# Performance work log

Measured on AMD Instinct MI355X. Metric: run time of the kernel, lower is better.

Reference implementation:

```python
import jax, jax.numpy as jnp
import numpy as np

NEG_INF = -9e15  # matches the torch module's zero_vec constant
ALPHA = 0.2      # LeakyReLU negative slope


def setup_inputs() -> dict:
    key = jax.random.key(0)
    k1, k2, k3, k4, k5, k6 = jax.random.split(key, 6)
    N_t, N_o, F_in, F_out = 8192, 8192, 256, 64
    return {
        "t_input": jax.random.normal(k1, (N_t, F_in), dtype=jnp.float32),
        "o_input": jax.random.normal(k2, (N_o, F_in), dtype=jnp.float32),
        "W_t": jax.random.normal(k3, (F_in, F_out), dtype=jnp.float32) * 0.1,
        "W_o": jax.random.normal(k4, (F_in, F_out), dtype=jnp.float32) * 0.1,
        "a": jax.random.normal(k5, (2 * F_out, 1), dtype=jnp.float32) * 0.1,
        "adj": jax.random.randint(k6, (N_t, N_o), 0, 2, dtype=jnp.int32),
    }


def reference(t_input, o_input, W_t, W_o, a, adj):
    # Linear projections
    h_t = t_input @ W_t            # [N_t, F]
    h_o = o_input @ W_o            # [N_o, F]
    F_out = h_t.shape[1]
    a_t = a[:F_out, 0]             # [F]
    a_o = a[F_out:, 0]             # [F]
    # e[i,j] = leakyrelu(cat(h_t[i], h_o[j]) . a) = leakyrelu(h_t[i].a_t + h_o[j].a_o)
    # (avoids materializing the N_t*N_o*2F concat tensor; same math)
    e = jax.nn.leaky_relu(
        (h_t @ a_t)[:, None] + (h_o @ a_o)[None, :], negative_slope=ALPHA
    )                              # [N_t, N_o]
    attention = jnp.where(adj > 0, e, NEG_INF)
    attention = jax.nn.softmax(attention, axis=1)
    # dropout is identity at eval time
    h_prime = attention @ h_o      # [N_t, F]
    return jax.nn.elu(h_prime)     # concat=True
```

## Files before the change

kernel.cpp:

```cpp
#include <hip/hip_runtime.h>
#include <math.h>

#define NT 8192
#define NO 8192
#define FIN 256
#define FOUT 64
#define SPLIT 8
#define JSP (NO/SPLIT)
#define ROWT 64
#define NW32 (NO/32)

#define OFF_ST  ((size_t)0)
#define OFF_SO  (OFF_ST + (size_t)NT)
#define OFF_WT  (OFF_SO + (size_t)NO)
#define OFF_WO  (OFF_WT + (size_t)FIN)
#define OFF_NUM (OFF_WO + (size_t)FIN)
#define OFF_DEN (OFF_NUM + (size_t)SPLIT*NT*FOUT)
#define OFF_HOB (OFF_DEN + (size_t)SPLIT*NT)
#define OFF_ETA (OFF_HOB + (size_t)NO*FOUT/2)
#define OFF_MSK (OFF_ETA + (size_t)NO*2)

typedef __attribute__((ext_vector_type(8))) short short8;
typedef __attribute__((ext_vector_type(4))) float float4v;

static __device__ __forceinline__ unsigned short f2bf(float x) {
  unsigned int u = __float_as_uint(x);
  unsigned int r = (u + 0x7fffu + ((u >> 16) & 1u)) >> 16;
  return (unsigned short)r;
}
static __device__ __forceinline__ int pk2(float a, float b) {
  return (int)((unsigned int)f2bf(a) | ((unsigned int)f2bf(b) << 16));
}
static __device__ __forceinline__ float bflo(int p) {
  return __uint_as_float(((unsigned int)p) << 16);
}
static __device__ __forceinline__ float bfhi(int p) {
  return __uint_as_float(((unsigned int)p) & 0xffff0000u);
}

__global__ void k_mask(const int* __restrict__ adj, float* __restrict__ ws) {
  unsigned int* mw = (unsigned int*)(ws + OFF_MSK);
  int wv = threadIdx.x >> 6, lane = threadIdx.x & 63;
  int gw = blockIdx.x * 4 + wv;
  const int NCH = NT*NO/256;
#pragma unroll 2
  for (int c = gw; c < NCH; c += 8192) {
    int4 a = *(const int4*)(adj + (size_t)c*256 + lane*4);
    unsigned int nib = (a.x > 0 ? 1u : 0u) | (a.y > 0 ? 2u : 0u)
                     | (a.z > 0 ? 4u : 0u) | (a.w > 0 ? 8u : 0u);
    unsigned int val = nib << ((lane & 7) * 4);
    val |= __shfl_xor((int)val, 1, 64);
    val |= __shfl_xor((int)val, 2, 64);
    val |= __shfl_xor((int)val, 4, 64);
    if ((lane & 7) == 0) mw[(size_t)c*8 + (lane >> 3)] = val;
  }
}

__global__ void k_wvec(const float* __restrict__ Wt, const float* __restrict__ Wo,
                       const float* __restrict__ a, float* __restrict__ ws) {
  int k = threadIdx.x;
  float s1 = 0.f, s2 = 0.f;
#pragma unroll
  for (int fq = 0; fq < FOUT/4; ++fq) {
    float4 wt4 = *(const float4*)(Wt + (size_t)k*FOUT + fq*4);
    float4 wo4 = *(const float4*)(Wo + (size_t)k*FOUT + fq*4);
    float4 at4 = *(const float4*)(a + fq*4);
    float4 ao4 = *(const float4*)(a + FOUT + fq*4);
    s1 += wt4.x*at4.x + wt4.y*at4.y + wt4.z*at4.z + wt4.w*at4.w;
    s2 += wo4.x*ao4.x + wo4.y*ao4.y + wo4.z*ao4.z + wo4.w*ao4.w;
  }
  ws[OFF_WT + k] = s1;
  ws[OFF_WO + k] = s2;
}

__global__ void k_st(const float* __restrict__ tin, float* __restrict__ ws) {
  int lane = threadIdx.x & 63;
  int wv   = threadIdx.x >> 6;
  int row  = blockIdx.x * 4 + wv;
  float4 v = ((const float4*)(tin + (size_t)row*FIN))[lane];
  float4 w = ((const float4*)(ws + OFF_WT))[lane];
  float p = v.x*w.x + v.y*w.y + v.z*w.z + v.w*w.w;
#pragma unroll
  for (int m = 32; m >= 1; m >>= 1) p += __shfl_xor(p, m, 64);
  if (lane == 0) ws[OFF_ST + row] = p;
}

__global__ void k_ho(const float* __restrict__ oin, const float* __restrict__ Wo,
                     const float* __restrict__ a, float* __restrict__ ws) {
  unsigned short* hobp = (unsigned short*)(ws + OFF_HOB);
  int lane = threadIdx.x & 63;
  int wv = __builtin_amdgcn_readfirstlane(threadIdx.x >> 6);
  int r0 = blockIdx.x * 16 + wv * 4;
  const float* ob = oin + (size_t)r0 * FIN;
  float acc[4];
#pragma unroll
  for (int r = 0; r < 4; ++r) acc[r] = 0.f;
#pragma unroll 2
  for (int k = 0; k < FIN; k += 4) {
    float w0 = Wo[(size_t)(k+0)*FOUT + lane];
    float w1 = Wo[(size_t)(k+1)*FOUT + lane];
    float w2 = Wo[(size_t)(k+2)*FOUT + lane];
    float w3 = Wo[(size_t)(k+3)*FOUT + lane];
#pragma unroll
    for (int r = 0; r < 4; ++r) {
      float4 ov = *(const float4*)(ob + (size_t)r*FIN + k);
      acc[r] = fmaf(ov.x, w0, acc[r]);
      acc[r] = fmaf(ov.y, w1, acc[r]);
      acc[r] = fmaf(ov.z, w2, acc[r]);
      acc[r] = fmaf(ov.w, w3, acc[r]);
    }
  }
  float ao = a[FOUT + lane];
  int fg = lane >> 4, n16 = lane & 15;
#pragma unroll
  for (int r = 0; r < 4; ++r) {
    int j = r0 + r;
    int jt = j >> 5, jl = j & 31;
    int ldst = (jl >> 3) * 16 + n16;
    int e = jl & 7;
    hobp[(((size_t)jt*4 + fg)*64 + ldst)*8 + e] = f2bf(acc[r]);
    float p = acc[r] * ao;
#pragma unroll
    for (int m = 32; m >= 1; m >>= 1) p += __shfl_xor(p, m, 64);
    if (lane == 0) ws[OFF_SO + j] = p;
  }
}

__global__ void k_etab(float* __restrict__ ws) {
  int j = blockIdx.x * 256 + threadIdx.x;
  float s = ws[OFF_SO + j];
  ws[OFF_ETA + 2*j + 0] = __expf(s);
  ws[OFF_ETA + 2*j + 1] = __expf(0.2f * s);
}

__launch_bounds__(256, 4)
__global__ void k_attn(float* __restrict__ ws) {
  const float* st = ws + OFF_ST;
  const float* etab = ws + OFF_ETA;
  const unsigned int* maskw = (const unsigned int*)(ws + OFF_MSK);
  const unsigned short* hobp = (const unsigned short*)(ws + OFF_HOB);
  float* gnum = ws + OFF_NUM;
  float* gden = ws + OFF_DEN;

  int t = threadIdx.x;
  int wv = t >> 6, lane = t & 63;
  int bx = blockIdx.x;
  int s  = bx & (SPLIT - 1);
  int bi = bx >> 3;
  int i0 = bi * ROWT;
  int jb = s * JSP;

  int rsrc = lane >> 2, csrc = lane & 3;
  int irow_s = i0 + wv*16 + rsrc;
  float sti  = st[irow_s];
  float esti  = __expf(sti);
  float esti2 = __expf(0.2f * sti);
  float ethr  = __expf(-sti);

  const unsigned int* mrow = maskw + (size_t)irow_s * NW32 + (jb >> 5);
  const float* ep = etab + (size_t)(jb + csrc*8) * 2;
  const unsigned short* hpb = hobp + (size_t)(jb >> 5) * 2048 + lane*8;

  int r16 = lane & 15, kg = lane >> 4;
  int sidx4 = ((r16 * 4 + kg) << 2);

  float4v acc0 = (float4v)0.f, acc1 = (float4v)0.f;
  float4v acc2 = (float4v)0.f, acc3 = (float4v)0.f;
  float dsum = 0.f;

#pragma unroll 1
  for (int tt = 0; tt < JSP/32; ++tt) {
    unsigned int mwv = mrow[tt];
    const float* e_ = ep + tt*64;
    float4 e0 = *(const float4*)(e_);
    float4 e1 = *(const float4*)(e_ + 4);
    float4 e2 = *(const float4*)(e_ + 8);
    float4 e3 = *(const float4*)(e_ + 12);
    const unsigned short* hb = hpb + (size_t)tt*2048;
    short8 b0 = *(const short8*)(hb);
    short8 b1 = *(const short8*)(hb + 512);
    short8 b2 = *(const short8*)(hb + 1024);
    short8 b3 = *(const short8*)(hb + 1536);

    unsigned int msh = mwv >> (csrc * 8);
    float w0 = ((e0.x >= ethr) ? esti*e0.x : esti2*e0.y); w0 = (msh & 1u)   ? w0 : 0.f;
    float w1 = ((e0.z >= ethr) ? esti*e0.z : esti2*e0.w); w1 = (msh & 2u)   ? w1 : 0.f;
    float w2 = ((e1.x >= ethr) ? esti*e1.x : esti2*e1.y); w2 = (msh & 4u)   ? w2 : 0.f;
    float w3 = ((e1.z >= ethr) ? esti*e1.z : esti2*e1.w); w3 = (msh & 8u)   ? w3 : 0.f;
    float w4 = ((e2.x >= ethr) ? esti*e2.x : esti2*e2.y); w4 = (msh & 16u)  ? w4 : 0.f;
    float w5 = ((e2.z >= ethr) ? esti*e2.z : esti2*e2.w); w5 = (msh & 32u)  ? w5 : 0.f;
    float w6 = ((e3.x >= ethr) ? esti*e3.x : esti2*e3.y); w6 = (msh & 64u)  ? w6 : 0.f;
    float w7 = ((e3.z >= ethr) ? esti*e3.z : esti2*e3.w); w7 = (msh & 128u) ? w7 : 0.f;

    int p0 = pk2(w0, w1);
    int p1 = pk2(w2, w3);
    int p2 = pk2(w4, w5);
    int p3 = pk2(w6, w7);
    dsum += bflo(p0) + bfhi(p0) + bflo(p1) + bfhi(p1)
          + bflo(p2) + bfhi(p2) + bflo(p3) + bfhi(p3);

    int4 ai;
    ai.x = __builtin_amdgcn_ds_bpermute(sidx4, p0);
    ai.y = __builtin_amdgcn_ds_bpermute(sidx4, p1);
    ai.z = __builtin_amdgcn_ds_bpermute(sidx4, p2);
    ai.w = __builtin_amdgcn_ds_bpermute(sidx4, p3);
    short8 afrag = *(short8*)&ai;

    acc0 = __builtin_amdgcn_mfma_f32_16x16x32_bf16(afrag, b0, acc0, 0, 0, 0);
    acc1 = __builtin_amdgcn_mfma_f32_16x16x32_bf16(afrag, b1, acc1, 0, 0, 0);
    acc2 = __builtin_amdgcn_mfma_f32_16x16x32_bf16(afrag, b2, acc2, 0, 0, 0);
    acc3 = __builtin_amdgcn_mfma_f32_16x16x32_bf16(afrag, b3, acc3, 0, 0, 0);
  }

  dsum += __shfl_xor(dsum, 1, 64);
  dsum += __shfl_xor(dsum, 2, 64);
  if (csrc == 0) gden[(size_t)s*NT + i0 + wv*16 + rsrc] = dsum;

  size_t obase = ((size_t)s*NT + i0 + wv*16 + kg*4) * FOUT + r16;
#pragma unroll
  for (int r = 0; r < 4; ++r) {
    gnum[obase + (size_t)r*FOUT +  0] = acc0[r];
    gnum[obase + (size_t)r*FOUT + 16] = acc1[r];
    gnum[obase + (size_t)r*FOUT + 32] = acc2[r];
    gnum[obase + (size_t)r*FOUT + 48] = acc3[r];
  }
}

__global__ void k_comb(const float* __restrict__ ws, float* __restrict__ out) {
  int idx = blockIdx.x * 256 + threadIdx.x;
  int i = idx >> 6;
  float num = 0.f, den = 0.f;
#pragma unroll
  for (int s = 0; s < SPLIT; ++s) {
    num += ws[OFF_NUM + ((size_t)s*NT + i)*FOUT + (idx & 63)];
    den += ws[OFF_DEN + (size_t)s*NT + i];
  }
  float r = num / den;
  out[idx] = (r > 0.f) ? r : (__expf(r) - 1.f);
}

extern "C" void kernel_launch(void* const* d_in, const int* in_sizes, int n_in,
                              void* d_out, int out_size, void* d_ws, size_t ws_size,
                              hipStream_t stream) {
  const float* tin = (const float*)d_in[0];
  const float* oin = (const float*)d_in[1];
  const float* Wt  = (const float*)d_in[2];
  const float* Wo  = (const float*)d_in[3];
  const float* a   = (const float*)d_in[4];
  const int*   adj = (const int*)d_in[5];
  float* out = (float*)d_out;
  float* ws  = (float*)d_ws;

  hipLaunchKernelGGL(k_mask, dim3(2048),           dim3(256), 0, stream, adj, ws);
  hipLaunchKernelGGL(k_wvec, dim3(1),              dim3(256), 0, stream, Wt, Wo, a, ws);
  hipLaunchKernelGGL(k_st,   dim3(NT/4),           dim3(256), 0, stream, tin, ws);
  hipLaunchKernelGGL(k_ho,   dim3(NO/16),          dim3(256), 0, stream, oin, Wo, a, ws);
  hipLaunchKernelGGL(k_etab, dim3(NO/256),         dim3(256), 0, stream, ws);
  hipLaunchKernelGGL(k_attn, dim3(NT/ROWT*SPLIT),  dim3(256), 0, stream, ws);
  hipLaunchKernelGGL(k_comb, dim3(NT*FOUT/256),    dim3(256), 0, stream, ws, out);
}
```

Before: 459.8 us.

## Fuse adjacency mask packing into attention kernel with prefetched int loads

```diff
diff --git a/kernel.cpp b/kernel.cpp
--- a/kernel.cpp
+++ b/kernel.cpp
@@ -8,7 +8,6 @@
 #define SPLIT 8
 #define JSP (NO/SPLIT)
 #define ROWT 64
-#define NW32 (NO/32)
 
 #define OFF_ST  ((size_t)0)
 #define OFF_SO  (OFF_ST + (size_t)NT)
@@ -18,7 +17,6 @@
 #define OFF_DEN (OFF_NUM + (size_t)SPLIT*NT*FOUT)
 #define OFF_HOB (OFF_DEN + (size_t)SPLIT*NT)
 #define OFF_ETA (OFF_HOB + (size_t)NO*FOUT/2)
-#define OFF_MSK (OFF_ETA + (size_t)NO*2)
 
 typedef __attribute__((ext_vector_type(8))) short short8;
 typedef __attribute__((ext_vector_type(4))) float float4v;
@@ -36,24 +34,6 @@
 }
 static __device__ __forceinline__ float bfhi(int p) {
   return __uint_as_float(((unsigned int)p) & 0xffff0000u);
-}
-
-__global__ void k_mask(const int* __restrict__ adj, float* __restrict__ ws) {
-  unsigned int* mw = (unsigned int*)(ws + OFF_MSK);
-  int wv = threadIdx.x >> 6, lane = threadIdx.x & 63;
-  int gw = blockIdx.x * 4 + wv;
-  const int NCH = NT*NO/256;
-#pragma unroll 2
-  for (int c = gw; c < NCH; c += 8192) {
-    int4 a = *(const int4*)(adj + (size_t)c*256 + lane*4);
-    unsigned int nib = (a.x > 0 ? 1u : 0u) | (a.y > 0 ? 2u : 0u)
-                     | (a.z > 0 ? 4u : 0u) | (a.w > 0 ? 8u : 0u);
-    unsigned int val = nib << ((lane & 7) * 4);
-    val |= __shfl_xor((int)val, 1, 64);
-    val |= __shfl_xor((int)val, 2, 64);
-    val |= __shfl_xor((int)val, 4, 64);
-    if ((lane & 7) == 0) mw[(size_t)c*8 + (lane >> 3)] = val;
-  }
 }
 
 __global__ void k_wvec(const float* __restrict__ Wt, const float* __restrict__ Wo,
@@ -134,10 +114,9 @@
 }
 
 __launch_bounds__(256, 4)
-__global__ void k_attn(float* __restrict__ ws) {
+__global__ void k_attn(const int* __restrict__ adj, float* __restrict__ ws) {
   const float* st = ws + OFF_ST;
   const float* etab = ws + OFF_ETA;
-  const unsigned int* maskw = (const unsigned int*)(ws + OFF_MSK);
   const unsigned short* hobp = (const unsigned short*)(ws + OFF_HOB);
   float* gnum = ws + OFF_NUM;
   float* gden = ws + OFF_DEN;
@@ -157,7 +136,7 @@
   float esti2 = __expf(0.2f * sti);
   float ethr  = __expf(-sti);
 
-  const unsigned int* mrow = maskw + (size_t)irow_s * NW32 + (jb >> 5);
+  const int* arow = adj + (size_t)irow_s * NO + jb + csrc*8;
   const float* ep = etab + (size_t)(jb + csrc*8) * 2;
   const unsigned short* hpb = hobp + (size_t)(jb >> 5) * 2048 + lane*8;
 
@@ -168,9 +147,15 @@
   float4v acc2 = (float4v)0.f, acc3 = (float4v)0.f;
   float dsum = 0.f;
 
+  int4 a0 = *(const int4*)(arow);
+  int4 a1 = *(const int4*)(arow + 4);
+
 #pragma unroll 1
   for (int tt = 0; tt < JSP/32; ++tt) {
-    unsigned int mwv = mrow[tt];
+    int ttn = (tt < JSP/32 - 1) ? tt + 1 : tt;
+    int4 n0 = *(const int4*)(arow + ttn*32);
+    int4 n1 = *(const int4*)(arow + ttn*32 + 4);
+
     const float* e_ = ep + tt*64;
     float4 e0 = *(const float4*)(e_);
     float4 e1 = *(const float4*)(e_ + 4);
@@ -182,15 +167,14 @@
     short8 b2 = *(const short8*)(hb + 1024);
     short8 b3 = *(const short8*)(hb + 1536);
 
-    unsigned int msh = mwv >> (csrc * 8);
-    float w0 = ((e0.x >= ethr) ? esti*e0.x : esti2*e0.y); w0 = (msh & 1u)   ? w0 : 0.f;
-    float w1 = ((e0.z >= ethr) ? esti*e0.z : esti2*e0.w); w1 = (msh & 2u)   ? w1 : 0.f;
-    float w2 = ((e1.x >= ethr) ? esti*e1.x : esti2*e1.y); w2 = (msh & 4u)   ? w2 : 0.f;
-    float w3 = ((e1.z >= ethr) ? esti*e1.z : esti2*e1.w); w3 = (msh & 8u)   ? w3 : 0.f;
-    float w4 = ((e2.x >= ethr) ? esti*e2.x : esti2*e2.y); w4 = (msh & 16u)  ? w4 : 0.f;
-    float w5 = ((e2.z >= ethr) ? esti*e2.z : esti2*e2.w); w5 = (msh & 32u)  ? w5 : 0.f;
-    float w6 = ((e3.x >= ethr) ? esti*e3.x : esti2*e3.y); w6 = (msh & 64u)  ? w6 : 0.f;
-    float w7 = ((e3.z >= ethr) ? esti*e3.z : esti2*e3.w); w7 = (msh & 128u) ? w7 : 0.f;
+    float w0 = ((e0.x >= ethr) ? esti*e0.x : esti2*e0.y); w0 = (a0.x > 0) ? w0 : 0.f;
+    float w1 = ((e0.z >= ethr) ? esti*e0.z : esti2*e0.w); w1 = (a0.y > 0) ? w1 : 0.f;
+    float w2 = ((e1.x >= ethr) ? esti*e1.x : esti2*e1.y); w2 = (a0.z > 0) ? w2 : 0.f;
+    float w3 = ((e1.z >= ethr) ? esti*e1.z : esti2*e1.w); w3 = (a0.w > 0) ? w3 : 0.f;
+    float w4 = ((e2.x >= ethr) ? esti*e2.x : esti2*e2.y); w4 = (a1.x > 0) ? w4 : 0.f;
+    float w5 = ((e2.z >= ethr) ? esti*e2.z : esti2*e2.w); w5 = (a1.y > 0) ? w5 : 0.f;
+    float w6 = ((e3.x >= ethr) ? esti*e3.x : esti2*e3.y); w6 = (a1.z > 0) ? w6 : 0.f;
+    float w7 = ((e3.z >= ethr) ? esti*e3.z : esti2*e3.w); w7 = (a1.w > 0) ? w7 : 0.f;
 
     int p0 = pk2(w0, w1);
     int p1 = pk2(w2, w3);
@@ -210,6 +194,8 @@
     acc1 = __builtin_amdgcn_mfma_f32_16x16x32_bf16(afrag, b1, acc1, 0, 0, 0);
     acc2 = __builtin_amdgcn_mfma_f32_16x16x32_bf16(afrag, b2, acc2, 0, 0, 0);
     acc3 = __builtin_amdgcn_mfma_f32_16x16x32_bf16(afrag, b3, acc3, 0, 0, 0);
+
+    a0 = n0; a1 = n1;
   }
 
   dsum += __shfl_xor(dsum, 1, 64);
@@ -251,11 +237,10 @@
   float* out = (float*)d_out;
   float* ws  = (float*)d_ws;
 
-  hipLaunchKernelGGL(k_mask, dim3(2048),           dim3(256), 0, stream, adj, ws);
   hipLaunchKernelGGL(k_wvec, dim3(1),              dim3(256), 0, stream, Wt, Wo, a, ws);
   hipLaunchKernelGGL(k_st,   dim3(NT/4),           dim3(256), 0, stream, tin, ws);
   hipLaunchKernelGGL(k_ho,   dim3(NO/16),          dim3(256), 0, stream, oin, Wo, a, ws);
   hipLaunchKernelGGL(k_etab, dim3(NO/256),         dim3(256), 0, stream, ws);
-  hipLaunchKernelGGL(k_attn, dim3(NT/ROWT*SPLIT),  dim3(256), 0, stream, ws);
+  hipLaunchKernelGGL(k_attn, dim3(NT/ROWT*SPLIT),  dim3(256), 0, stream, adj, ws);
   hipLaunchKernelGGL(k_comb, dim3(NT*FOUT/256),    dim3(256), 0, stream, ws, out);
 }
```

New measurement: 449.6 us. 2.2% less time.
